# Kernel tuning notes

Measured on AMD Instinct MI355X. Metric: run time of the kernel, lower is better.

## Reference

```python
import jax, jax.numpy as jnp
import numpy as np

K = 512       # knowledge_n = node count AND feature dim
S = 50000     # student_n
E_N = 6       # exer_n (hardcoded as literal 6 in the original forward)
DEG_K = 4     # exercise neighbors per knowledge node
DEG_S = 3     # exercise neighbors per student
NEG_SLOPE = 0.2  # PyG GATConv default


def setup_inputs() -> dict:
    key = jax.random.key(0)
    ks = jax.random.split(key, 10)
    kn_emb = jax.random.normal(ks[0], (K, K), jnp.float32)
    exer_emb = jax.random.normal(ks[1], (E_N, K), jnp.float32)
    all_stu_emb = jax.random.normal(ks[2], (S, K), jnp.float32)
    # k_from_e graph: nodes = [exercises(0..5), knowledge(6..6+K-1)]
    src_ke = jax.random.randint(ks[3], (K * DEG_K,), 0, E_N)
    dst_ke = E_N + jnp.repeat(jnp.arange(K), DEG_K)
    edges_ke = jnp.stack([src_ke, dst_ke]).astype(jnp.int32)   # e -> k
    edges_ek = edges_ke[::-1]                                  # k -> e
    # u_from_e graph: nodes = [exercises(0..5), students(6..6+S-1)]
    src_ue = jax.random.randint(ks[4], (S * DEG_S,), 0, E_N)
    dst_ue = E_N + jnp.repeat(jnp.arange(S), DEG_S)
    edges_ue = jnp.stack([src_ue, dst_ue]).astype(jnp.int32)   # e -> u
    edges_eu = edges_ue[::-1]                                  # u -> e
    sc = 1.0 / np.sqrt(K)
    W_gat = jax.random.normal(ks[5], (4, K, K), jnp.float32) * sc
    a_src = jax.random.normal(ks[6], (4, K), jnp.float32) * sc
    a_dst = jax.random.normal(ks[7], (4, K), jnp.float32) * sc
    b_gat = jnp.zeros((4, K), jnp.float32)
    attn_w = jax.random.normal(ks[8], (3, 2 * K), jnp.float32) / np.sqrt(2 * K)
    attn_b = jnp.zeros((3,), jnp.float32)
    return dict(kn_emb=kn_emb, exer_emb=exer_emb, all_stu_emb=all_stu_emb,
                W_gat=W_gat, a_src=a_src, a_dst=a_dst, b_gat=b_gat,
                attn_w=attn_w, attn_b=attn_b,
                edges_ke=edges_ke, edges_ek=edges_ek,
                edges_ue=edges_ue, edges_eu=edges_eu)


def _gat(x, edges, W, a_s, a_d, b, n):
    """Single-head PyG GATConv with self-loops. edges[0]=src, edges[1]=dst."""
    h = x @ W                                   # [n, K]
    loop = jnp.arange(n, dtype=edges.dtype)
    src = jnp.concatenate([edges[0], loop])
    dst = jnp.concatenate([edges[1], loop])
    alpha_s = h @ a_s                           # [n]
    alpha_d = h @ a_d
    e = jax.nn.leaky_relu(alpha_s[src] + alpha_d[dst], NEG_SLOPE)
    emax = jax.lax.stop_gradient(jax.ops.segment_max(e, dst, num_segments=n))
    ex = jnp.exp(e - emax[dst])
    den = jax.ops.segment_sum(ex, dst, num_segments=n)
    alpha = ex / den[dst]                       # per-dst softmax
    out = jax.ops.segment_sum(alpha[:, None] * h[src], dst, num_segments=n)
    return out + b


def reference(kn_emb, exer_emb, all_stu_emb, W_gat, a_src, a_dst, b_gat,
              attn_w, attn_b, edges_ke, edges_ek, edges_ue, edges_eu):
    e_k = jnp.concatenate([exer_emb, kn_emb], axis=0)        # [6+K, K]
    e_u = jnp.concatenate([exer_emb, all_stu_emb], axis=0)   # [6+S, K]
    n_ek, n_eu = e_k.shape[0], e_u.shape[0]
    k_from_e = _gat(e_k, edges_ke, W_gat[0], a_src[0], a_dst[0], b_gat[0], n_ek)
    e_from_k = _gat(e_k, edges_ek, W_gat[1], a_src[1], a_dst[1], b_gat[1], n_ek)
    u_from_e = _gat(e_u, edges_ue, W_gat[2], a_src[2], a_dst[2], b_gat[2], n_eu)
    e_from_u = _gat(e_u, edges_eu, W_gat[3], a_src[3], a_dst[3], b_gat[3], n_eu)
    # knowledge fusion (softmax over a single column -> all ones, kept faithful)
    D = k_from_e[E_N:]
    s3 = jnp.concatenate([kn_emb, D], axis=1) @ attn_w[0] + attn_b[0]   # [K]
    sc = jax.nn.softmax(s3[:, None], axis=1)
    kn_out = kn_emb + sc[:, 0:1] * D
    # exercise fusion: 2-way attention over knowledge/student messages
    B = e_from_k[:E_N]
    C = e_from_u[:E_N]
    s1 = jnp.concatenate([exer_emb, B], axis=1) @ attn_w[1] + attn_b[1]
    s2 = jnp.concatenate([exer_emb, C], axis=1) @ attn_w[2] + attn_b[2]
    sc2 = jax.nn.softmax(jnp.stack([s1, s2], axis=1), axis=1)           # [6, 2]
    exer_out = exer_emb + sc2[:, 0:1] * B + sc2[:, 1:2] * C
    stu_out = all_stu_emb + u_from_e[E_N:]
    return (kn_out, exer_out, stu_out)
```

## Files before the change

kernel.cpp:

```cpp
#include <hip/hip_runtime.h>

typedef __attribute__((ext_vector_type(4))) float f4;
typedef __attribute__((ext_vector_type(8))) short s8;

__device__ __forceinline__ unsigned short f2bf(float x){
  unsigned u = __float_as_uint(x);
  u += 0x7fffu + ((u >> 16) & 1u);
  return (unsigned short)(u >> 16);
}
__device__ __forceinline__ float lrelu(float v){ return v > 0.f ? v : 0.2f * v; }

__device__ __forceinline__ void gload16(const unsigned short* g, unsigned short* l){
  __builtin_amdgcn_global_load_lds((const __attribute__((address_space(1))) unsigned int*)g,
                                   (__attribute__((address_space(3))) unsigned int*)l, 16, 0, 0);
}

__global__ void prep_pq(const float* __restrict__ Wg, const float* __restrict__ a_src,
                        const float* __restrict__ a_dst, float* __restrict__ pq,
                        float* __restrict__ zbase){
  int tid = blockIdx.x * 256 + threadIdx.x;
  for (int i = tid; i < 6156; i += gridDim.x * 256) zbase[i] = 0.f;
  int wid = tid >> 6, lane = tid & 63;
  for (int task = wid; task < 4096; task += gridDim.x * 4){
    int g = task >> 10, isq = (task >> 9) & 1, r = task & 511;
    const float* w = Wg + ((g * 512 + r) << 9);
    const float* a = (isq ? a_dst : a_src) + g * 512;
    float s = 0.f;
    for (int i = lane; i < 512; i += 64) s += w[i] * a[i];
    for (int off = 32; off; off >>= 1) s += __shfl_down(s, off);
    if (lane == 0) pq[task] = s;
  }
}

__global__ void prep_wt(const float* __restrict__ Wg, unsigned short* __restrict__ W2T,
                        unsigned short* __restrict__ W0T){
  __shared__ float tile[32][33];
  const int b = blockIdx.x;
  const int m = b >> 8;
  const int kb = (b & 15) * 32;
  const int nb = ((b >> 4) & 15) * 32;
  const float* W = Wg + (m == 0 ? 2 * 262144 : 0);
  unsigned short* WT = (m == 0) ? W2T : W0T;
  const int tx = threadIdx.x & 31, ty = threadIdx.x >> 5;
  #pragma unroll
  for (int i = 0; i < 32; i += 8) tile[ty + i][tx] = W[(kb + ty + i) * 512 + nb + tx];
  __syncthreads();
  #pragma unroll
  for (int i = 0; i < 32; i += 8) WT[(nb + ty + i) * 512 + kb + tx] = f2bf(tile[tx][ty + i]);
}

__global__ void prep_he(const float* __restrict__ exer, const float* __restrict__ Wg,
                        const float* __restrict__ pq, float* __restrict__ asE,
                        float* __restrict__ adE, float* __restrict__ HE2,
                        float* __restrict__ HE0){
  const int b = blockIdx.x;
  const int g = (b < 6) ? 0 : 2;
  const int e = b % 6;
  __shared__ float xs[512];
  const int t = threadIdx.x;
  xs[t] = exer[e * 512 + t];
  __syncthreads();
  const int wid = t >> 6, lane = t & 63;
  if (wid < 4){
    int gg = g + (wid >> 1), isq = wid & 1;
    const float* v = pq + gg * 1024 + isq * 512;
    float s = 0.f;
    for (int i = lane; i < 512; i += 64) s += xs[i] * v[i];
    for (int off = 32; off; off >>= 1) s += __shfl_down(s, off);
    if (lane == 0) (isq ? adE : asE)[gg * 6 + e] = s;
  }
  const float* W = Wg + g * 262144;
  float acc = 0.f;
  for (int k = 0; k < 512; k++) acc += xs[k] * W[k * 512 + t];
  ((g == 0) ? HE0 : HE2)[e * 512 + t] = acc;
}

template<int DEG>
__launch_bounds__(256)
__global__ void pass1(const float* __restrict__ x, const float* __restrict__ pq,
                      int gA, int gB,
                      const float* __restrict__ asE, const float* __restrict__ adE,
                      float* __restrict__ alph, const int* __restrict__ idx,
                      float* __restrict__ Craw, float* __restrict__ den, int M)
{
  __shared__ float sC[3072];
  __shared__ float sDen[6];
  const int tid = threadIdx.x, lane = tid & 63, wid = tid >> 6;
  for (int i = tid; i < 3072; i += 256) sC[i] = 0.f;
  if (tid < 6) sDen[tid] = 0.f;

  const int kb = lane * 8;
  const float* pqA = pq + gA * 1024;
  const float* pqB = pq + gB * 1024;
  f4 pA0 = *(const f4*)(pqA + kb),       pA1 = *(const f4*)(pqA + kb + 4);
  f4 qA0 = *(const f4*)(pqA + 512 + kb), qA1 = *(const f4*)(pqA + 512 + kb + 4);
  f4 pB0 = *(const f4*)(pqB + kb),       pB1 = *(const f4*)(pqB + kb + 4);
  float aseR = asE[gA * 6 + (lane % 6)];
  float adeR = adE[gB * 6 + (lane % 6)];

  float cacc[6][8];
  #pragma unroll
  for (int e = 0; e < 6; e++)
    #pragma unroll
    for (int i = 0; i < 8; i++) cacc[e][i] = 0.f;
  float dacc[6] = {0.f,0.f,0.f,0.f,0.f,0.f};
  __syncthreads();

  const int gw = blockIdx.x * 4 + wid, nw = gridDim.x * 4;
  for (int r = gw; r < M; r += nw){
    const float* xr = x + (size_t)r * 512;
    f4 x0 = *(const f4*)(xr + kb), x1 = *(const f4*)(xr + kb + 4);
    float dP = 0.f, dQ = 0.f, dB = 0.f;
    #pragma unroll
    for (int i = 0; i < 4; i++){
      dP += x0[i]*pA0[i] + x1[i]*pA1[i];
      dQ += x0[i]*qA0[i] + x1[i]*qA1[i];
      dB += x0[i]*pB0[i] + x1[i]*pB1[i];
    }
    #pragma unroll
    for (int off = 1; off < 64; off <<= 1){
      dP += __shfl_xor(dP, off); dQ += __shfl_xor(dQ, off); dB += __shfl_xor(dB, off);
    }
    int ei[DEG];
    #pragma unroll
    for (int j = 0; j < DEG; j++) ei[j] = idx[r * DEG + j];
    float scS = lrelu(dP + dQ);
    float sc[DEG], m = scS;
    #pragma unroll
    for (int j = 0; j < DEG; j++){ sc[j] = lrelu(__shfl(aseR, ei[j]) + dQ); m = fmaxf(m, sc[j]); }
    float eS = __expf(scS - m), sum = eS;
    float ev[DEG];
    #pragma unroll
    for (int j = 0; j < DEG; j++){ ev[j] = __expf(sc[j] - m); sum += ev[j]; }
    float inv = 1.f / sum;
    float val = 0.f;
    if (lane == 0) val = eS * inv;
    else if (lane < 7){
      #pragma unroll
      for (int j = 0; j < DEG; j++) val += (ei[j] == lane - 1) ? ev[j] * inv : 0.f;
    }
    if (lane < 8) alph[(size_t)r * 8 + lane] = val;
    float wj[DEG];
    #pragma unroll
    for (int j = 0; j < DEG; j++) wj[j] = __expf(lrelu(dB + __shfl(adeR, ei[j])));
    #pragma unroll
    for (int e = 0; e < 6; e++){
      float we = 0.f;
      #pragma unroll
      for (int j = 0; j < DEG; j++) we += (ei[j] == e) ? wj[j] : 0.f;
      dacc[e] += we;
      #pragma unroll
      for (int i = 0; i < 4; i++){ cacc[e][i] += we * x0[i]; cacc[e][4+i] += we * x1[i]; }
    }
  }
  #pragma unroll
  for (int e = 0; e < 6; e++)
    #pragma unroll
    for (int i = 0; i < 8; i++)
      atomicAdd(&sC[e * 512 + kb + i], cacc[e][i]);
  if (lane == 0){
    #pragma unroll
    for (int e = 0; e < 6; e++) atomicAdd(&sDen[e], dacc[e]);
  }
  __syncthreads();
  for (int i = tid; i < 3072; i += 256){
    float v = sC[i];
    if (v != 0.f) atomicAdd(&Craw[i], v);
  }
  if (tid < 6) atomicAdd(&den[tid], sDen[tid]);
}

__launch_bounds__(256, 2)
__global__ void gemm_ep(const float* __restrict__ x, const unsigned short* __restrict__ WT,
                        const float* __restrict__ alph, const float* __restrict__ HE,
                        const float* __restrict__ bA, float* __restrict__ outp, int M)
{
  __shared__ __align__(16) unsigned short sA[4096];
  __shared__ __align__(16) unsigned short sB[4096];
  __shared__ __align__(16) float sAl[1024];
  __shared__ __align__(16) float sHEb[768];
  __shared__ __align__(16) float sB2[128];

  const int nwg = gridDim.x;
  const int q = nwg >> 3, rr = nwg & 7, xcd = blockIdx.x & 7, pos = blockIdx.x >> 3;
  const int wid = (xcd < rr ? xcd * (q + 1) : rr * (q + 1) + (xcd - rr) * q) + pos;
  const int mb = wid >> 2, nb = wid & 3;
  const int r0 = mb * 128, n0 = nb * 128;
  const int tid = threadIdx.x, lane = tid & 63, w = tid >> 6;
  const int wr = w >> 1, wc = w & 1, l16 = lane & 15, lhi = lane >> 4;

  { int row = min(r0 + (tid >> 1), M - 1);
    *(f4*)(sAl + tid * 4) = *(const f4*)(alph + (size_t)row * 8 + (tid & 1) * 4); }
  if (tid < 192) *(f4*)(sHEb + tid * 4) = *(const f4*)(HE + (tid >> 5) * 512 + n0 + (tid & 31) * 4);
  else if (tid < 224) *(f4*)(sB2 + (tid - 192) * 4) = *(const f4*)(bA + n0 + (tid - 192) * 4);

  const int sRow = tid >> 2, sK = (tid & 3) * 8;
  const float* xA0 = x + (size_t)min(r0 + sRow, M - 1) * 512 + sK;
  const float* xA1 = x + (size_t)min(r0 + 64 + sRow, M - 1) * 512 + sK;
  const unsigned short* gB0 = WT + (size_t)(n0 + sRow) * 512 + sK;
  const unsigned short* gB1 = WT + (size_t)(n0 + 64 + sRow) * 512 + sK;
  unsigned short* lA0 = sA + sRow * 32 + sK;
  unsigned short* lA1 = sA + (64 + sRow) * 32 + sK;
  unsigned short* lB0 = sB + sRow * 32 + sK;
  unsigned short* lB1 = sB + (64 + sRow) * 32 + sK;

  f4 acc[4][4];
  #pragma unroll
  for (int m = 0; m < 4; m++)
    #pragma unroll
    for (int n = 0; n < 4; n++) acc[m][n] = (f4){0.f, 0.f, 0.f, 0.f};

  f4 n00 = *(const f4*)(xA0),     n01 = *(const f4*)(xA0 + 4);
  f4 n10 = *(const f4*)(xA1),     n11 = *(const f4*)(xA1 + 4);

  for (int kt = 0; kt < 16; kt++){
    const int ko = kt * 32;
    gload16(gB0 + ko, lB0);
    gload16(gB1 + ko, lB1);
    s8 p0, p1;
    #pragma unroll
    for (int i = 0; i < 4; i++){
      p0[i]   = (short)f2bf(n00[i]); p0[4+i] = (short)f2bf(n01[i]);
      p1[i]   = (short)f2bf(n10[i]); p1[4+i] = (short)f2bf(n11[i]);
    }
    *(s8*)lA0 = p0; *(s8*)lA1 = p1;
    if (kt < 15){
      n00 = *(const f4*)(xA0 + ko + 32); n01 = *(const f4*)(xA0 + ko + 36);
      n10 = *(const f4*)(xA1 + ko + 32); n11 = *(const f4*)(xA1 + ko + 36);
    }
    __syncthreads();
    s8 af[4], bfr[4];
    #pragma unroll
    for (int m = 0; m < 4; m++) af[m] = *(const s8*)(sA + (wr * 64 + m * 16 + l16) * 32 + lhi * 8);
    #pragma unroll
    for (int n = 0; n < 4; n++) bfr[n] = *(const s8*)(sB + (wc * 64 + n * 16 + l16) * 32 + lhi * 8);
    #pragma unroll
    for (int m = 0; m < 4; m++)
      #pragma unroll
      for (int n = 0; n < 4; n++)
        acc[m][n] = __builtin_amdgcn_mfma_f32_16x16x32_bf16(af[m], bfr[n], acc[m][n], 0, 0, 0);
    __syncthreads();
  }

  #pragma unroll
  for (int m = 0; m < 4; m++){
    const int rl = wr * 64 + m * 16 + lhi * 4;
    #pragma unroll
    for (int n = 0; n < 4; n++){
      const int cl = wc * 64 + n * 16 + l16;
      const int gc = n0 + cl;
      const float hb = sB2[cl];
      #pragma unroll
      for (int j = 0; j < 4; j++){
        const int row = r0 + rl + j;
        if (row < M){
          const float* al = sAl + (rl + j) * 8;
          float v = x[(size_t)row * 512 + gc] + al[0] * acc[m][n][j] + hb;
          #pragma unroll
          for (int e = 0; e < 6; e++) v += al[1 + e] * sHEb[e * 128 + cl];
          outp[(size_t)row * 512 + gc] = v;
        }
      }
    }
  }
}

__global__ void finalize_bc(const float* __restrict__ exer, const float* __restrict__ Wg,
                            const float* __restrict__ asE, const float* __restrict__ adE,
                            const float* __restrict__ Craw3, const float* __restrict__ den3,
                            const float* __restrict__ Craw1, const float* __restrict__ den1,
                            const float* __restrict__ b_gat, float* __restrict__ B,
                            float* __restrict__ C){
  const int b = blockIdx.x;
  const int isC = (b >= 6) ? 1 : 0;
  const int e = b % 6;
  const int g = isC ? 3 : 1;
  const float* Craw = isC ? Craw3 : Craw1;
  const float* den  = isC ? den3  : den1;
  __shared__ float mix[512];
  const int t = threadIdx.x;
  float aS = asE[g*6 + e], aD = adE[g*6 + e];
  float wself = __expf(lrelu(aS + aD));
  float dn = den[e] + wself;
  mix[t] = (Craw[e*512 + t] + wself * exer[e*512 + t]) / dn;
  __syncthreads();
  const float* W = Wg + g * 262144;
  float acc = 0.f;
  for (int k = 0; k < 512; k++) acc += mix[k] * W[k*512 + t];
  acc += b_gat[g*512 + t];
  (isC ? C : B)[e*512 + t] = acc;
}

__global__ void finalize_exer(const float* __restrict__ exer, const float* __restrict__ B,
                              const float* __restrict__ C, const float* __restrict__ attn_w,
                              const float* __restrict__ attn_b, float* __restrict__ outE){
  __shared__ float s1[6], s2[6];
  const int t = threadIdx.x, wid = t >> 6, lane = t & 63;
  for (int task = wid; task < 12; task += 8){
    int e = task >> 1, which = task & 1;
    const float* w = attn_w + (which + 1) * 1024;
    const float* X = exer + e * 512;
    const float* Y = (which ? C : B) + e * 512;
    float s = 0.f;
    for (int i = lane; i < 512; i += 64) s += X[i] * w[i] + Y[i] * w[512 + i];
    for (int off = 32; off; off >>= 1) s += __shfl_down(s, off);
    if (lane == 0) (which ? s2 : s1)[e] = s + attn_b[which + 1];
  }
  __syncthreads();
  for (int i = t; i < 3072; i += 512){
    int e = i >> 9;
    float a = s1[e], b = s2[e];
    float m = fmaxf(a, b);
    float ea = __expf(a - m), eb = __expf(b - m);
    float inv = 1.f / (ea + eb);
    outE[i] = exer[i] + (ea * inv) * B[i] + (eb * inv) * C[i];
  }
}

extern "C" void kernel_launch(void* const* d_in, const int* in_sizes, int n_in,
                              void* d_out, int out_size, void* d_ws, size_t ws_size,
                              hipStream_t stream){
  const float* kn     = (const float*)d_in[0];
  const float* exer   = (const float*)d_in[1];
  const float* stu    = (const float*)d_in[2];
  const float* Wg     = (const float*)d_in[3];
  const float* a_src  = (const float*)d_in[4];
  const float* a_dst  = (const float*)d_in[5];
  const float* b_gat  = (const float*)d_in[6];
  const float* attn_w = (const float*)d_in[7];
  const float* attn_b = (const float*)d_in[8];
  const int*   e_ke   = (const int*)d_in[9];
  const int*   e_ue   = (const int*)d_in[11];
  float* out = (float*)d_out;

  unsigned short* W2T = (unsigned short*)d_ws;
  unsigned short* W0T = W2T + 262144;
  float* pq    = (float*)(W0T + 262144);
  float* asE   = pq + 4096;
  float* adE   = asE + 24;
  float* HE2   = adE + 24;
  float* HE0   = HE2 + 3072;
  float* Craw3 = HE0 + 3072;
  float* Craw1 = Craw3 + 3072;
  float* den3  = Craw1 + 3072;
  float* den1  = den3 + 6;
  float* Bb    = den1 + 6;
  float* Cc    = Bb + 3072;
  float* alphS = Cc + 3072;
  float* alphK = alphS + 400000;

  hipLaunchKernelGGL(prep_pq, dim3(256), dim3(256), 0, stream, Wg, a_src, a_dst, pq, Craw3);
  hipLaunchKernelGGL(prep_wt, dim3(512), dim3(256), 0, stream, Wg, W2T, W0T);
  hipLaunchKernelGGL(prep_he, dim3(12), dim3(512), 0, stream, exer, Wg, pq, asE, adE, HE2, HE0);

  hipLaunchKernelGGL((pass1<3>), dim3(768), dim3(256), 0, stream,
                     stu, pq, 2, 3, asE, adE, alphS, e_ue, Craw3, den3, 50000);
  hipLaunchKernelGGL((pass1<4>), dim3(8), dim3(256), 0, stream,
                     kn, pq, 0, 1, asE, adE, alphK, e_ke, Craw1, den1, 512);

  hipLaunchKernelGGL(gemm_ep, dim3(1564), dim3(256), 0, stream,
                     stu, W2T, alphS, HE2, b_gat + 1024, out + 265216, 50000);
  hipLaunchKernelGGL(gemm_ep, dim3(16), dim3(256), 0, stream,
                     kn, W0T, alphK, HE0, b_gat, out, 512);

  hipLaunchKernelGGL(finalize_bc, dim3(12), dim3(512), 0, stream,
                     exer, Wg, asE, adE, Craw3, den3, Craw1, den1, b_gat, Bb, Cc);
  hipLaunchKernelGGL(finalize_exer, dim3(1), dim3(512), 0, stream,
                     exer, Bb, Cc, attn_w, attn_b, out + 262144);
}
```

Measured before the change: 474.7 us.

## Restructure GEMM to keep full weight tile in LDS and split-K small matvecs

The main GEMM now loads a 64-column slice of the transposed bf16 weight (full K=512) into swizzled LDS once per block. Each of 8 waves streams its own 16 rows of activations straight from global memory, so the per-k-step syncs and the A-tile staging go away. The tile becomes 128x64 with 512 threads. The small exercise matvecs in prep_he and finalize_bc are split across 8 K-chunks with atomic accumulation, and a separate prep_scal kernel computes the attention scalars. The zeroed workspace region is enlarged to cover the new atomic targets. Costs include 64KB of LDS per block limiting occupancy, each activation row being read by 8 column blocks, and atomics that make summation order nondeterministic.

```diff
diff --git a/kernel.cpp b/kernel.cpp
--- a/kernel.cpp
+++ b/kernel.cpp
@@ -19,7 +19,7 @@
                         const float* __restrict__ a_dst, float* __restrict__ pq,
                         float* __restrict__ zbase){
   int tid = blockIdx.x * 256 + threadIdx.x;
-  for (int i = tid; i < 6156; i += gridDim.x * 256) zbase[i] = 0.f;
+  for (int i = tid; i < 18444; i += gridDim.x * 256) zbase[i] = 0.f;
   int wid = tid >> 6, lane = tid & 63;
   for (int task = wid; task < 4096; task += gridDim.x * 4){
     int g = task >> 10, isq = (task >> 9) & 1, r = task & 511;
@@ -49,30 +49,35 @@
   for (int i = 0; i < 32; i += 8) WT[(nb + ty + i) * 512 + kb + tx] = f2bf(tile[tx][ty + i]);
 }
 
+__global__ void prep_scal(const float* __restrict__ exer, const float* __restrict__ pq,
+                          float* __restrict__ asE, float* __restrict__ adE){
+  const int t = threadIdx.x, wid = t >> 6, lane = t & 63;
+  for (int task = wid; task < 48; task += 4){
+    int gg = task / 12, rem = task % 12, isq = rem / 6, e = rem % 6;
+    const float* X = exer + e * 512;
+    const float* V = pq + gg * 1024 + isq * 512;
+    float s = 0.f;
+    for (int i = lane; i < 512; i += 64) s += X[i] * V[i];
+    for (int off = 32; off; off >>= 1) s += __shfl_down(s, off);
+    if (lane == 0) (isq ? adE : asE)[gg * 6 + e] = s;
+  }
+}
+
 __global__ void prep_he(const float* __restrict__ exer, const float* __restrict__ Wg,
-                        const float* __restrict__ pq, float* __restrict__ asE,
-                        float* __restrict__ adE, float* __restrict__ HE2,
-                        float* __restrict__ HE0){
+                        float* __restrict__ HE2, float* __restrict__ HE0){
   const int b = blockIdx.x;
+  const int ks = blockIdx.y;
   const int g = (b < 6) ? 0 : 2;
   const int e = b % 6;
-  __shared__ float xs[512];
+  __shared__ float xs[64];
   const int t = threadIdx.x;
-  xs[t] = exer[e * 512 + t];
-  __syncthreads();
-  const int wid = t >> 6, lane = t & 63;
-  if (wid < 4){
-    int gg = g + (wid >> 1), isq = wid & 1;
-    const float* v = pq + gg * 1024 + isq * 512;
-    float s = 0.f;
-    for (int i = lane; i < 512; i += 64) s += xs[i] * v[i];
-    for (int off = 32; off; off >>= 1) s += __shfl_down(s, off);
-    if (lane == 0) (isq ? adE : asE)[gg * 6 + e] = s;
-  }
-  const float* W = Wg + g * 262144;
+  if (t < 64) xs[t] = exer[e * 512 + ks * 64 + t];
+  __syncthreads();
+  const float* W = Wg + g * 262144 + ks * 64 * 512;
   float acc = 0.f;
-  for (int k = 0; k < 512; k++) acc += xs[k] * W[k * 512 + t];
-  ((g == 0) ? HE0 : HE2)[e * 512 + t] = acc;
+  #pragma unroll 4
+  for (int kk = 0; kk < 64; kk++) acc += xs[kk] * W[kk * 512 + t];
+  atomicAdd(&((g == 0) ? HE0 : HE2)[e * 512 + t], acc);
 }
 
 template<int DEG>
@@ -170,96 +175,91 @@
   if (tid < 6) atomicAdd(&den[tid], sDen[tid]);
 }
 
-__launch_bounds__(256, 2)
+__launch_bounds__(512, 4)
 __global__ void gemm_ep(const float* __restrict__ x, const unsigned short* __restrict__ WT,
                         const float* __restrict__ alph, const float* __restrict__ HE,
                         const float* __restrict__ bA, float* __restrict__ outp, int M)
 {
-  __shared__ __align__(16) unsigned short sA[4096];
-  __shared__ __align__(16) unsigned short sB[4096];
+  __shared__ __align__(16) unsigned short sB[32768];
   __shared__ __align__(16) float sAl[1024];
-  __shared__ __align__(16) float sHEb[768];
-  __shared__ __align__(16) float sB2[128];
+  __shared__ __align__(16) float sHEb[384];
+  __shared__ __align__(16) float sBias[64];
 
   const int nwg = gridDim.x;
-  const int q = nwg >> 3, rr = nwg & 7, xcd = blockIdx.x & 7, pos = blockIdx.x >> 3;
-  const int wid = (xcd < rr ? xcd * (q + 1) : rr * (q + 1) + (xcd - rr) * q) + pos;
-  const int mb = wid >> 2, nb = wid & 3;
-  const int r0 = mb * 128, n0 = nb * 128;
+  const int xcd = blockIdx.x & 7, pos = blockIdx.x >> 3;
+  const int wido = xcd * (nwg >> 3) + pos;
+  const int mb = wido >> 3, nb = wido & 7;
+  const int r0 = mb * 128, n0 = nb * 64;
   const int tid = threadIdx.x, lane = tid & 63, w = tid >> 6;
-  const int wr = w >> 1, wc = w & 1, l16 = lane & 15, lhi = lane >> 4;
-
-  { int row = min(r0 + (tid >> 1), M - 1);
-    *(f4*)(sAl + tid * 4) = *(const f4*)(alph + (size_t)row * 8 + (tid & 1) * 4); }
-  if (tid < 192) *(f4*)(sHEb + tid * 4) = *(const f4*)(HE + (tid >> 5) * 512 + n0 + (tid & 31) * 4);
-  else if (tid < 224) *(f4*)(sB2 + (tid - 192) * 4) = *(const f4*)(bA + n0 + (tid - 192) * 4);
-
-  const int sRow = tid >> 2, sK = (tid & 3) * 8;
-  const float* xA0 = x + (size_t)min(r0 + sRow, M - 1) * 512 + sK;
-  const float* xA1 = x + (size_t)min(r0 + 64 + sRow, M - 1) * 512 + sK;
-  const unsigned short* gB0 = WT + (size_t)(n0 + sRow) * 512 + sK;
-  const unsigned short* gB1 = WT + (size_t)(n0 + 64 + sRow) * 512 + sK;
-  unsigned short* lA0 = sA + sRow * 32 + sK;
-  unsigned short* lA1 = sA + (64 + sRow) * 32 + sK;
-  unsigned short* lB0 = sB + sRow * 32 + sK;
-  unsigned short* lB1 = sB + (64 + sRow) * 32 + sK;
-
-  f4 acc[4][4];
-  #pragma unroll
-  for (int m = 0; m < 4; m++)
-    #pragma unroll
-    for (int n = 0; n < 4; n++) acc[m][n] = (f4){0.f, 0.f, 0.f, 0.f};
-
-  f4 n00 = *(const f4*)(xA0),     n01 = *(const f4*)(xA0 + 4);
-  f4 n10 = *(const f4*)(xA1),     n11 = *(const f4*)(xA1 + 4);
-
+  const int l16 = lane & 15, lhi = lane >> 4;
+
+  {
+    const int row = (tid >> 6), slot = tid & 63;
+    #pragma unroll
+    for (int it = 0; it < 8; it++){
+      const int rr = it * 8 + row;
+      const unsigned short* src = WT + (size_t)(n0 + rr) * 512 + ((slot ^ (rr & 7)) << 3);
+      gload16(src, sB + it * 4096 + tid * 8);
+    }
+  }
+  if (tid < 256){
+    const int row = tid >> 1;
+    *(f4*)(sAl + tid * 4) = *(const f4*)(alph + (size_t)min(r0 + row, M - 1) * 8 + (tid & 1) * 4);
+  } else if (tid < 352){
+    const int idx2 = tid - 256, e = idx2 >> 4, c4 = idx2 & 15;
+    *(f4*)(sHEb + e * 64 + c4 * 4) = *(const f4*)(HE + e * 512 + n0 + c4 * 4);
+  } else if (tid < 368){
+    const int idx2 = tid - 352;
+    *(f4*)(sBias + idx2 * 4) = *(const f4*)(bA + n0 + idx2 * 4);
+  }
+  __syncthreads();
+
+  const int gr0 = r0 + w * 16 + l16;
+  const float* xr = x + (size_t)min(gr0, M - 1) * 512 + lhi * 8;
+
+  f4 acc[4];
+  #pragma unroll
+  for (int n = 0; n < 4; n++) acc[n] = (f4){0.f, 0.f, 0.f, 0.f};
+
+  #pragma unroll 4
   for (int kt = 0; kt < 16; kt++){
-    const int ko = kt * 32;
-    gload16(gB0 + ko, lB0);
-    gload16(gB1 + ko, lB1);
-    s8 p0, p1;
-    #pragma unroll
-    for (int i = 0; i < 4; i++){
-      p0[i]   = (short)f2bf(n00[i]); p0[4+i] = (short)f2bf(n01[i]);
-      p1[i]   = (short)f2bf(n10[i]); p1[4+i] = (short)f2bf(n11[i]);
-    }
-    *(s8*)lA0 = p0; *(s8*)lA1 = p1;
-    if (kt < 15){
-      n00 = *(const f4*)(xA0 + ko + 32); n01 = *(const f4*)(xA0 + ko + 36);
-      n10 = *(const f4*)(xA1 + ko + 32); n11 = *(const f4*)(xA1 + ko + 36);
-    }
-    __syncthreads();
-    s8 af[4], bfr[4];
-    #pragma unroll
-    for (int m = 0; m < 4; m++) af[m] = *(const s8*)(sA + (wr * 64 + m * 16 + l16) * 32 + lhi * 8);
-    #pragma unroll
-    for (int n = 0; n < 4; n++) bfr[n] = *(const s8*)(sB + (wc * 64 + n * 16 + l16) * 32 + lhi * 8);
-    #pragma unroll
-    for (int m = 0; m < 4; m++)
+    f4 a0 = *(const f4*)(xr + kt * 32);
+    f4 a1 = *(const f4*)(xr + kt * 32 + 4);
+    s8 af;
+    #pragma unroll
+    for (int i = 0; i < 4; i++){ af[i] = (short)f2bf(a0[i]); af[4+i] = (short)f2bf(a1[i]); }
+    #pragma unroll
+    for (int n = 0; n < 4; n++){
+      const int row = n * 16 + l16;
+      const int slot = ((kt << 2) + lhi) ^ (row & 7);
+      s8 bf = *(const s8*)(sB + row * 512 + (slot << 3));
+      acc[n] = __builtin_amdgcn_mfma_f32_16x16x32_bf16(af, bf, acc[n], 0, 0, 0);
+    }
+  }
+
+  float hec[4][6], bias[4];
+  #pragma unroll
+  for (int n = 0; n < 4; n++){
+    bias[n] = sBias[n * 16 + l16];
+    #pragma unroll
+    for (int e = 0; e < 6; e++) hec[n][e] = sHEb[e * 64 + n * 16 + l16];
+  }
+
+  #pragma unroll
+  for (int j = 0; j < 4; j++){
+    const int rl = w * 16 + lhi * 4 + j;
+    const int gr = r0 + rl;
+    if (gr < M){
+      f4 alA = *(const f4*)(sAl + rl * 8);
+      f4 alB = *(const f4*)(sAl + rl * 8 + 4);
+      const float aself = alA[0];
       #pragma unroll
-      for (int n = 0; n < 4; n++)
-        acc[m][n] = __builtin_amdgcn_mfma_f32_16x16x32_bf16(af[m], bfr[n], acc[m][n], 0, 0, 0);
-    __syncthreads();
-  }
-
-  #pragma unroll
-  for (int m = 0; m < 4; m++){
-    const int rl = wr * 64 + m * 16 + lhi * 4;
-    #pragma unroll
-    for (int n = 0; n < 4; n++){
-      const int cl = wc * 64 + n * 16 + l16;
-      const int gc = n0 + cl;
-      const float hb = sB2[cl];
-      #pragma unroll
-      for (int j = 0; j < 4; j++){
-        const int row = r0 + rl + j;
-        if (row < M){
-          const float* al = sAl + (rl + j) * 8;
-          float v = x[(size_t)row * 512 + gc] + al[0] * acc[m][n][j] + hb;
-          #pragma unroll
-          for (int e = 0; e < 6; e++) v += al[1 + e] * sHEb[e * 128 + cl];
-          outp[(size_t)row * 512 + gc] = v;
-        }
+      for (int n = 0; n < 4; n++){
+        const int gc = n0 + n * 16 + l16;
+        float v = x[(size_t)gr * 512 + gc] + aself * acc[n][j] + bias[n];
+        v += alA[1] * hec[n][0] + alA[2] * hec[n][1] + alA[3] * hec[n][2];
+        v += alB[0] * hec[n][3] + alB[1] * hec[n][4] + alB[2] * hec[n][5];
+        outp[(size_t)gr * 512 + gc] = v;
       }
     }
   }
@@ -272,23 +272,28 @@
                             const float* __restrict__ b_gat, float* __restrict__ B,
                             float* __restrict__ C){
   const int b = blockIdx.x;
+  const int ks = blockIdx.y;
   const int isC = (b >= 6) ? 1 : 0;
   const int e = b % 6;
   const int g = isC ? 3 : 1;
   const float* Craw = isC ? Craw3 : Craw1;
   const float* den  = isC ? den3  : den1;
-  __shared__ float mix[512];
+  __shared__ float mix[64];
   const int t = threadIdx.x;
   float aS = asE[g*6 + e], aD = adE[g*6 + e];
   float wself = __expf(lrelu(aS + aD));
   float dn = den[e] + wself;
-  mix[t] = (Craw[e*512 + t] + wself * exer[e*512 + t]) / dn;
-  __syncthreads();
-  const float* W = Wg + g * 262144;
+  if (t < 64){
+    int k = ks * 64 + t;
+    mix[t] = (Craw[e*512 + k] + wself * exer[e*512 + k]) / dn;
+  }
+  __syncthreads();
+  const float* W = Wg + g * 262144 + ks * 64 * 512;
   float acc = 0.f;
-  for (int k = 0; k < 512; k++) acc += mix[k] * W[k*512 + t];
-  acc += b_gat[g*512 + t];
-  (isC ? C : B)[e*512 + t] = acc;
+  #pragma unroll 4
+  for (int kk = 0; kk < 64; kk++) acc += mix[kk] * W[kk * 512 + t];
+  if (ks == 0) acc += b_gat[g*512 + t];
+  atomicAdd(&(isC ? C : B)[e*512 + t], acc);
 }
 
 __global__ void finalize_exer(const float* __restrict__ exer, const float* __restrict__ B,
@@ -335,35 +340,37 @@
 
   unsigned short* W2T = (unsigned short*)d_ws;
   unsigned short* W0T = W2T + 262144;
-  float* pq    = (float*)(W0T + 262144);
+  float* fb    = (float*)(W0T + 262144);
+  float* pq    = fb;
   float* asE   = pq + 4096;
   float* adE   = asE + 24;
-  float* HE2   = adE + 24;
-  float* HE0   = HE2 + 3072;
-  float* Craw3 = HE0 + 3072;
+  float* Craw3 = adE + 24;
   float* Craw1 = Craw3 + 3072;
   float* den3  = Craw1 + 3072;
   float* den1  = den3 + 6;
-  float* Bb    = den1 + 6;
+  float* HE2   = den1 + 6;
+  float* HE0   = HE2 + 3072;
+  float* Bb    = HE0 + 3072;
   float* Cc    = Bb + 3072;
   float* alphS = Cc + 3072;
-  float* alphK = alphS + 400000;
+  float* alphK = alphS + 400384;
 
   hipLaunchKernelGGL(prep_pq, dim3(256), dim3(256), 0, stream, Wg, a_src, a_dst, pq, Craw3);
   hipLaunchKernelGGL(prep_wt, dim3(512), dim3(256), 0, stream, Wg, W2T, W0T);
-  hipLaunchKernelGGL(prep_he, dim3(12), dim3(512), 0, stream, exer, Wg, pq, asE, adE, HE2, HE0);
+  hipLaunchKernelGGL(prep_scal, dim3(1), dim3(256), 0, stream, exer, pq, asE, adE);
+  hipLaunchKernelGGL(prep_he, dim3(12, 8), dim3(512), 0, stream, exer, Wg, HE2, HE0);
 
   hipLaunchKernelGGL((pass1<3>), dim3(768), dim3(256), 0, stream,
                      stu, pq, 2, 3, asE, adE, alphS, e_ue, Craw3, den3, 50000);
   hipLaunchKernelGGL((pass1<4>), dim3(8), dim3(256), 0, stream,
                      kn, pq, 0, 1, asE, adE, alphK, e_ke, Craw1, den1, 512);
 
-  hipLaunchKernelGGL(gemm_ep, dim3(1564), dim3(256), 0, stream,
+  hipLaunchKernelGGL(gemm_ep, dim3(391 * 8), dim3(512), 0, stream,
                      stu, W2T, alphS, HE2, b_gat + 1024, out + 265216, 50000);
-  hipLaunchKernelGGL(gemm_ep, dim3(16), dim3(256), 0, stream,
+  hipLaunchKernelGGL(gemm_ep, dim3(4 * 8), dim3(512), 0, stream,
                      kn, W0T, alphK, HE0, b_gat, out, 512);
 
-  hipLaunchKernelGGL(finalize_bc, dim3(12), dim3(512), 0, stream,
+  hipLaunchKernelGGL(finalize_bc, dim3(12, 8), dim3(512), 0, stream,
                      exer, Wg, asE, adE, Craw3, den3, Craw1, den1, b_gat, Bb, Cc);
   hipLaunchKernelGGL(finalize_exer, dim3(1), dim3(512), 0, stream,
                      exer, Bb, Cc, attn_w, attn_b, out + 262144);
```

Result: slower. 485.2 us (+2.2%).

## Merge prep, pass1 and GEMM launches; double-buffer and swizzle GEMM LDS

Applied to the files above, without the earlier changes.

Three prep kernels become one multi-role kernel, the two pass1 launches become one, and the two GEMM launches become one, which cuts launch count from nine to five. The GEMM now double-buffers its A and B tiles with XOR-swizzled LDS offsets, so there is one barrier per k-step and fewer bank conflicts. It also raises occupancy bounds to 3 blocks per CU and hoists the epilogue HE and bias values into registers. Exercise attention scalars are recomputed inside pass1 and fin_bc, and fin_bc is split over K with atomics, which relies on B and C being zeroed by the prep kernel.

```diff
diff --git a/kernel.cpp b/kernel.cpp
--- a/kernel.cpp
+++ b/kernel.cpp
@@ -9,85 +9,77 @@
   return (unsigned short)(u >> 16);
 }
 __device__ __forceinline__ float lrelu(float v){ return v > 0.f ? v : 0.2f * v; }
-
 __device__ __forceinline__ void gload16(const unsigned short* g, unsigned short* l){
   __builtin_amdgcn_global_load_lds((const __attribute__((address_space(1))) unsigned int*)g,
                                    (__attribute__((address_space(3))) unsigned int*)l, 16, 0, 0);
 }
 
-__global__ void prep_pq(const float* __restrict__ Wg, const float* __restrict__ a_src,
-                        const float* __restrict__ a_dst, float* __restrict__ pq,
-                        float* __restrict__ zbase){
-  int tid = blockIdx.x * 256 + threadIdx.x;
-  for (int i = tid; i < 6156; i += gridDim.x * 256) zbase[i] = 0.f;
-  int wid = tid >> 6, lane = tid & 63;
-  for (int task = wid; task < 4096; task += gridDim.x * 4){
-    int g = task >> 10, isq = (task >> 9) & 1, r = task & 511;
-    const float* w = Wg + ((g * 512 + r) << 9);
-    const float* a = (isq ? a_dst : a_src) + g * 512;
+__global__ __launch_bounds__(256) void prep(const float* __restrict__ Wg,
+    const float* __restrict__ a_src, const float* __restrict__ a_dst,
+    const float* __restrict__ exer, float* __restrict__ pq, float* __restrict__ zbase,
+    unsigned short* __restrict__ W2T, unsigned short* __restrict__ W0T,
+    float* __restrict__ HE2, float* __restrict__ HE0)
+{
+  __shared__ float tile[32][33];
+  __shared__ float xs[512];
+  const int b = blockIdx.x, t = threadIdx.x;
+  if (b < 512){
+    const int m = b >> 8, kb = (b & 15) * 32, nb = ((b >> 4) & 15) * 32;
+    const float* W = Wg + (m == 0 ? 2 * 262144 : 0);
+    unsigned short* WT = (m == 0) ? W2T : W0T;
+    const int tx = t & 31, ty = t >> 5;
+    #pragma unroll
+    for (int i = 0; i < 32; i += 8) tile[ty + i][tx] = W[(kb + ty + i) * 512 + nb + tx];
+    __syncthreads();
+    #pragma unroll
+    for (int i = 0; i < 32; i += 8) WT[(nb + ty + i) * 512 + kb + tx] = f2bf(tile[tx][ty + i]);
+  } else if (b < 768){
+    const int tid = (b - 512) * 256 + t;
+    if (tid < 12304) zbase[tid] = 0.f;
+    const int wid = tid >> 6, lane = tid & 63;
+    for (int task = wid; task < 4096; task += 1024){
+      int g = task >> 10, isq = (task >> 9) & 1, r = task & 511;
+      const float* w = Wg + ((g * 512 + r) << 9);
+      const float* a = (isq ? a_dst : a_src) + g * 512;
+      float s = 0.f;
+      for (int i = lane; i < 512; i += 64) s += w[i] * a[i];
+      for (int off = 32; off; off >>= 1) s += __shfl_down(s, off);
+      if (lane == 0) pq[task] = s;
+    }
+  } else {
+    const int b3 = b - 768;
+    const int g = (b3 < 6) ? 0 : 2, e = b3 % 6;
+    xs[t] = exer[e * 512 + t]; xs[t + 256] = exer[e * 512 + 256 + t];
+    __syncthreads();
+    const float* W = Wg + g * 262144;
+    float a0 = 0.f, a1 = 0.f;
+    #pragma unroll 8
+    for (int k = 0; k < 512; k++){ float xv = xs[k]; a0 += xv * W[k * 512 + t]; a1 += xv * W[k * 512 + 256 + t]; }
+    float* HE = (g == 0) ? HE0 : HE2;
+    HE[e * 512 + t] = a0; HE[e * 512 + 256 + t] = a1;
+  }
+}
+
+template<int DEG>
+__device__ void pass1_body(float* sC, float* sDen, float* sASE, float* sADE,
+                           int bid, int nblk, const float* __restrict__ x,
+                           const float* __restrict__ exer, const float* __restrict__ pq,
+                           int gA, int gB, const int* __restrict__ idx,
+                           float* __restrict__ alph, float* __restrict__ Craw,
+                           float* __restrict__ den, int M)
+{
+  const int t = threadIdx.x, lane = t & 63, w = t >> 6;
+  for (int i = t; i < 3072; i += 256) sC[i] = 0.f;
+  if (t < 6) sDen[t] = 0.f;
+  for (int d = w * 3; d < w * 3 + 3; d++){
+    const float* X = exer + (d % 6) * 512;
+    const float* V = (d < 6) ? (pq + gA * 1024) : (pq + gB * 1024 + 512);
     float s = 0.f;
-    for (int i = lane; i < 512; i += 64) s += w[i] * a[i];
+    for (int i = lane; i < 512; i += 64) s += X[i] * V[i];
     for (int off = 32; off; off >>= 1) s += __shfl_down(s, off);
-    if (lane == 0) pq[task] = s;
-  }
-}
-
-__global__ void prep_wt(const float* __restrict__ Wg, unsigned short* __restrict__ W2T,
-                        unsigned short* __restrict__ W0T){
-  __shared__ float tile[32][33];
-  const int b = blockIdx.x;
-  const int m = b >> 8;
-  const int kb = (b & 15) * 32;
-  const int nb = ((b >> 4) & 15) * 32;
-  const float* W = Wg + (m == 0 ? 2 * 262144 : 0);
-  unsigned short* WT = (m == 0) ? W2T : W0T;
-  const int tx = threadIdx.x & 31, ty = threadIdx.x >> 5;
-  #pragma unroll
-  for (int i = 0; i < 32; i += 8) tile[ty + i][tx] = W[(kb + ty + i) * 512 + nb + tx];
-  __syncthreads();
-  #pragma unroll
-  for (int i = 0; i < 32; i += 8) WT[(nb + ty + i) * 512 + kb + tx] = f2bf(tile[tx][ty + i]);
-}
-
-__global__ void prep_he(const float* __restrict__ exer, const float* __restrict__ Wg,
-                        const float* __restrict__ pq, float* __restrict__ asE,
-                        float* __restrict__ adE, float* __restrict__ HE2,
-                        float* __restrict__ HE0){
-  const int b = blockIdx.x;
-  const int g = (b < 6) ? 0 : 2;
-  const int e = b % 6;
-  __shared__ float xs[512];
-  const int t = threadIdx.x;
-  xs[t] = exer[e * 512 + t];
-  __syncthreads();
-  const int wid = t >> 6, lane = t & 63;
-  if (wid < 4){
-    int gg = g + (wid >> 1), isq = wid & 1;
-    const float* v = pq + gg * 1024 + isq * 512;
-    float s = 0.f;
-    for (int i = lane; i < 512; i += 64) s += xs[i] * v[i];
-    for (int off = 32; off; off >>= 1) s += __shfl_down(s, off);
-    if (lane == 0) (isq ? adE : asE)[gg * 6 + e] = s;
-  }
-  const float* W = Wg + g * 262144;
-  float acc = 0.f;
-  for (int k = 0; k < 512; k++) acc += xs[k] * W[k * 512 + t];
-  ((g == 0) ? HE0 : HE2)[e * 512 + t] = acc;
-}
-
-template<int DEG>
-__launch_bounds__(256)
-__global__ void pass1(const float* __restrict__ x, const float* __restrict__ pq,
-                      int gA, int gB,
-                      const float* __restrict__ asE, const float* __restrict__ adE,
-                      float* __restrict__ alph, const int* __restrict__ idx,
-                      float* __restrict__ Craw, float* __restrict__ den, int M)
-{
-  __shared__ float sC[3072];
-  __shared__ float sDen[6];
-  const int tid = threadIdx.x, lane = tid & 63, wid = tid >> 6;
-  for (int i = tid; i < 3072; i += 256) sC[i] = 0.f;
-  if (tid < 6) sDen[tid] = 0.f;
+    if (lane == 0) ((d < 6) ? sASE : sADE)[d % 6] = s;
+  }
+  __syncthreads();
 
   const int kb = lane * 8;
   const float* pqA = pq + gA * 1024;
@@ -95,8 +87,8 @@
   f4 pA0 = *(const f4*)(pqA + kb),       pA1 = *(const f4*)(pqA + kb + 4);
   f4 qA0 = *(const f4*)(pqA + 512 + kb), qA1 = *(const f4*)(pqA + 512 + kb + 4);
   f4 pB0 = *(const f4*)(pqB + kb),       pB1 = *(const f4*)(pqB + kb + 4);
-  float aseR = asE[gA * 6 + (lane % 6)];
-  float adeR = adE[gB * 6 + (lane % 6)];
+  const float aseR = sASE[lane % 6];
+  const float adeR = sADE[lane % 6];
 
   float cacc[6][8];
   #pragma unroll
@@ -104,9 +96,8 @@
     #pragma unroll
     for (int i = 0; i < 8; i++) cacc[e][i] = 0.f;
   float dacc[6] = {0.f,0.f,0.f,0.f,0.f,0.f};
-  __syncthreads();
-
-  const int gw = blockIdx.x * 4 + wid, nw = gridDim.x * 4;
+
+  const int gw = bid * 4 + w, nw = nblk * 4;
   for (int r = gw; r < M; r += nw){
     const float* xr = x + (size_t)r * 512;
     f4 x0 = *(const f4*)(xr + kb), x1 = *(const f4*)(xr + kb + 4);
@@ -163,46 +154,102 @@
     for (int e = 0; e < 6; e++) atomicAdd(&sDen[e], dacc[e]);
   }
   __syncthreads();
-  for (int i = tid; i < 3072; i += 256){
+  for (int i = t; i < 3072; i += 256){
     float v = sC[i];
     if (v != 0.f) atomicAdd(&Craw[i], v);
   }
-  if (tid < 6) atomicAdd(&den[tid], sDen[tid]);
-}
-
-__launch_bounds__(256, 2)
-__global__ void gemm_ep(const float* __restrict__ x, const unsigned short* __restrict__ WT,
-                        const float* __restrict__ alph, const float* __restrict__ HE,
-                        const float* __restrict__ bA, float* __restrict__ outp, int M)
-{
-  __shared__ __align__(16) unsigned short sA[4096];
-  __shared__ __align__(16) unsigned short sB[4096];
+  if (t < 6) atomicAdd(&den[t], sDen[t]);
+}
+
+__global__ __launch_bounds__(256) void pass1_all(const float* __restrict__ stu,
+    const float* __restrict__ kn, const float* __restrict__ exer,
+    const float* __restrict__ pq, const int* __restrict__ e_ue, const int* __restrict__ e_ke,
+    float* __restrict__ alphS, float* __restrict__ alphK,
+    float* __restrict__ Craw3, float* __restrict__ Craw1,
+    float* __restrict__ den3, float* __restrict__ den1)
+{
+  __shared__ float sC[3072];
+  __shared__ float sDen[6], sASE[6], sADE[6];
+  if (blockIdx.x < 768)
+    pass1_body<3>(sC, sDen, sASE, sADE, blockIdx.x, 768, stu, exer, pq, 2, 3,
+                  e_ue, alphS, Craw3, den3, 50000);
+  else
+    pass1_body<4>(sC, sDen, sASE, sADE, blockIdx.x - 768, 8, kn, exer, pq, 0, 1,
+                  e_ke, alphK, Craw1, den1, 512);
+}
+
+__launch_bounds__(256, 3)
+__global__ void gemm_all(const float* __restrict__ stu, const float* __restrict__ kn,
+                         const unsigned short* __restrict__ W2T, const unsigned short* __restrict__ W0T,
+                         const float* __restrict__ alphS, const float* __restrict__ alphK,
+                         const float* __restrict__ HE2, const float* __restrict__ HE0,
+                         const float* __restrict__ b_gat, float* __restrict__ outS,
+                         float* __restrict__ outK)
+{
+  __shared__ __align__(16) unsigned short sA[8192];
+  __shared__ __align__(16) unsigned short sB[8192];
   __shared__ __align__(16) float sAl[1024];
   __shared__ __align__(16) float sHEb[768];
-  __shared__ __align__(16) float sB2[128];
+  __shared__ __align__(16) float sBias[128];
 
   const int nwg = gridDim.x;
-  const int q = nwg >> 3, rr = nwg & 7, xcd = blockIdx.x & 7, pos = blockIdx.x >> 3;
-  const int wid = (xcd < rr ? xcd * (q + 1) : rr * (q + 1) + (xcd - rr) * q) + pos;
-  const int mb = wid >> 2, nb = wid & 3;
+  const int q = nwg >> 3, rr = nwg & 7;
+  const int xcd = blockIdx.x & 7, pos = blockIdx.x >> 3;
+  const int wido = (xcd < rr ? xcd * (q + 1) : rr * (q + 1) + (xcd - rr) * q) + pos;
+
+  const float* x; const unsigned short* WT; const float* alph; const float* HE;
+  const float* bias; float* outp; int M, mb, nb;
+  if (wido < 1564){
+    x = stu; WT = W2T; alph = alphS; HE = HE2; bias = b_gat + 1024; outp = outS; M = 50000;
+    mb = wido >> 2; nb = wido & 3;
+  } else {
+    const int w2 = wido - 1564;
+    x = kn; WT = W0T; alph = alphK; HE = HE0; bias = b_gat; outp = outK; M = 512;
+    mb = w2 >> 2; nb = w2 & 3;
+  }
   const int r0 = mb * 128, n0 = nb * 128;
   const int tid = threadIdx.x, lane = tid & 63, w = tid >> 6;
   const int wr = w >> 1, wc = w & 1, l16 = lane & 15, lhi = lane >> 4;
 
-  { int row = min(r0 + (tid >> 1), M - 1);
-    *(f4*)(sAl + tid * 4) = *(const f4*)(alph + (size_t)row * 8 + (tid & 1) * 4); }
+  const int arow = tid >> 1, akh = (tid & 1) * 16;
+  const float* aptr = x + (size_t)min(r0 + arow, M - 1) * 512 + akh;
+  const int akey = (arow >> 1) & 3, s0 = (tid & 1) * 2;
+  const int dA0 = arow * 32 + ((s0 ^ akey) << 3);
+  const int dA1 = arow * 32 + (((s0 + 1) ^ akey) << 3);
+
+  const int brow = tid >> 2, bslot = tid & 3;
+  const int bkey = (brow >> 1) & 3;
+  const unsigned short* gB0 = WT + (size_t)(n0 + brow) * 512 + ((bslot ^ bkey) << 3);
+  const unsigned short* gB1 = gB0 + (size_t)64 * 512;
+  unsigned short* lB0 = sB + tid * 8;
+  unsigned short* lB1 = sB + 2048 + tid * 8;
+
+  int aoff[4], boff[4];
+  #pragma unroll
+  for (int m = 0; m < 4; m++){
+    const int ra = wr * 64 + m * 16 + l16;
+    aoff[m] = ra * 32 + ((lhi ^ ((ra >> 1) & 3)) << 3);
+    const int rb = wc * 64 + m * 16 + l16;
+    boff[m] = rb * 32 + ((lhi ^ ((rb >> 1) & 3)) << 3);
+  }
+
+  gload16(gB0, lB0); gload16(gB1, lB1);
+  f4 c0 = *(const f4*)(aptr),     c1 = *(const f4*)(aptr + 4);
+  f4 c2 = *(const f4*)(aptr + 8), c3 = *(const f4*)(aptr + 12);
+  {
+    s8 p0, p1;
+    #pragma unroll
+    for (int i = 0; i < 4; i++){
+      p0[i] = (short)f2bf(c0[i]); p0[4+i] = (short)f2bf(c1[i]);
+      p1[i] = (short)f2bf(c2[i]); p1[4+i] = (short)f2bf(c3[i]);
+    }
+    *(s8*)(sA + dA0) = p0; *(s8*)(sA + dA1) = p1;
+  }
+  { const int rw = min(r0 + (tid >> 1), M - 1);
+    *(f4*)(sAl + tid * 4) = *(const f4*)(alph + (size_t)rw * 8 + (tid & 1) * 4); }
   if (tid < 192) *(f4*)(sHEb + tid * 4) = *(const f4*)(HE + (tid >> 5) * 512 + n0 + (tid & 31) * 4);
-  else if (tid < 224) *(f4*)(sB2 + (tid - 192) * 4) = *(const f4*)(bA + n0 + (tid - 192) * 4);
-
-  const int sRow = tid >> 2, sK = (tid & 3) * 8;
-  const float* xA0 = x + (size_t)min(r0 + sRow, M - 1) * 512 + sK;
-  const float* xA1 = x + (size_t)min(r0 + 64 + sRow, M - 1) * 512 + sK;
-  const unsigned short* gB0 = WT + (size_t)(n0 + sRow) * 512 + sK;
-  const unsigned short* gB1 = WT + (size_t)(n0 + 64 + sRow) * 512 + sK;
-  unsigned short* lA0 = sA + sRow * 32 + sK;
-  unsigned short* lA1 = sA + (64 + sRow) * 32 + sK;
-  unsigned short* lB0 = sB + sRow * 32 + sK;
-  unsigned short* lB1 = sB + (64 + sRow) * 32 + sK;
+  else if (tid < 224){ const int i2 = tid - 192; *(f4*)(sBias + i2 * 4) = *(const f4*)(bias + n0 + i2 * 4); }
+  __syncthreads();
 
   f4 acc[4][4];
   #pragma unroll
@@ -210,90 +257,111 @@
     #pragma unroll
     for (int n = 0; n < 4; n++) acc[m][n] = (f4){0.f, 0.f, 0.f, 0.f};
 
-  f4 n00 = *(const f4*)(xA0),     n01 = *(const f4*)(xA0 + 4);
-  f4 n10 = *(const f4*)(xA1),     n11 = *(const f4*)(xA1 + 4);
-
+  int bufo = 0;
+  #pragma unroll 1
   for (int kt = 0; kt < 16; kt++){
-    const int ko = kt * 32;
-    gload16(gB0 + ko, lB0);
-    gload16(gB1 + ko, lB1);
-    s8 p0, p1;
-    #pragma unroll
-    for (int i = 0; i < 4; i++){
-      p0[i]   = (short)f2bf(n00[i]); p0[4+i] = (short)f2bf(n01[i]);
-      p1[i]   = (short)f2bf(n10[i]); p1[4+i] = (short)f2bf(n11[i]);
-    }
-    *(s8*)lA0 = p0; *(s8*)lA1 = p1;
+    const int nxt = bufo ^ 4096;
     if (kt < 15){
-      n00 = *(const f4*)(xA0 + ko + 32); n01 = *(const f4*)(xA0 + ko + 36);
-      n10 = *(const f4*)(xA1 + ko + 32); n11 = *(const f4*)(xA1 + ko + 36);
-    }
-    __syncthreads();
-    s8 af[4], bfr[4];
-    #pragma unroll
-    for (int m = 0; m < 4; m++) af[m] = *(const s8*)(sA + (wr * 64 + m * 16 + l16) * 32 + lhi * 8);
-    #pragma unroll
-    for (int n = 0; n < 4; n++) bfr[n] = *(const s8*)(sB + (wc * 64 + n * 16 + l16) * 32 + lhi * 8);
+      gload16(gB0 + (kt + 1) * 32, lB0 + nxt);
+      gload16(gB1 + (kt + 1) * 32, lB1 + nxt);
+      c0 = *(const f4*)(aptr + (kt + 1) * 32);     c1 = *(const f4*)(aptr + (kt + 1) * 32 + 4);
+      c2 = *(const f4*)(aptr + (kt + 1) * 32 + 8); c3 = *(const f4*)(aptr + (kt + 1) * 32 + 12);
+    }
+    s8 af[4], bf[4];
+    #pragma unroll
+    for (int m = 0; m < 4; m++) af[m] = *(const s8*)(sA + bufo + aoff[m]);
+    #pragma unroll
+    for (int n = 0; n < 4; n++) bf[n] = *(const s8*)(sB + bufo + boff[n]);
     #pragma unroll
     for (int m = 0; m < 4; m++)
       #pragma unroll
       for (int n = 0; n < 4; n++)
-        acc[m][n] = __builtin_amdgcn_mfma_f32_16x16x32_bf16(af[m], bfr[n], acc[m][n], 0, 0, 0);
+        acc[m][n] = __builtin_amdgcn_mfma_f32_16x16x32_bf16(af[m], bf[n], acc[m][n], 0, 0, 0);
+    if (kt < 15){
+      s8 p0, p1;
+      #pragma unroll
+      for (int i = 0; i < 4; i++){
+        p0[i] = (short)f2bf(c0[i]); p0[4+i] = (short)f2bf(c1[i]);
+        p1[i] = (short)f2bf(c2[i]); p1[4+i] = (short)f2bf(c3[i]);
+      }
+      *(s8*)(sA + nxt + dA0) = p0; *(s8*)(sA + nxt + dA1) = p1;
+    }
     __syncthreads();
-  }
-
+    bufo = nxt;
+  }
+
+  float hec[4][6], bi[4];
+  #pragma unroll
+  for (int n = 0; n < 4; n++){
+    const int cl = wc * 64 + n * 16 + l16;
+    bi[n] = sBias[cl];
+    #pragma unroll
+    for (int e = 0; e < 6; e++) hec[n][e] = sHEb[e * 128 + cl];
+  }
   #pragma unroll
   for (int m = 0; m < 4; m++){
-    const int rl = wr * 64 + m * 16 + lhi * 4;
-    #pragma unroll
-    for (int n = 0; n < 4; n++){
-      const int cl = wc * 64 + n * 16 + l16;
-      const int gc = n0 + cl;
-      const float hb = sB2[cl];
-      #pragma unroll
-      for (int j = 0; j < 4; j++){
-        const int row = r0 + rl + j;
-        if (row < M){
-          const float* al = sAl + (rl + j) * 8;
-          float v = x[(size_t)row * 512 + gc] + al[0] * acc[m][n][j] + hb;
-          #pragma unroll
-          for (int e = 0; e < 6; e++) v += al[1 + e] * sHEb[e * 128 + cl];
-          outp[(size_t)row * 512 + gc] = v;
+    #pragma unroll
+    for (int j = 0; j < 4; j++){
+      const int rl = wr * 64 + m * 16 + lhi * 4 + j;
+      const int gr = r0 + rl;
+      if (gr < M){
+        f4 alA = *(const f4*)(sAl + rl * 8);
+        f4 alB = *(const f4*)(sAl + rl * 8 + 4);
+        #pragma unroll
+        for (int n = 0; n < 4; n++){
+          const int gc = n0 + wc * 64 + n * 16 + l16;
+          float v = x[(size_t)gr * 512 + gc] + alA[0] * acc[m][n][j] + bi[n];
+          v += alA[1] * hec[n][0] + alA[2] * hec[n][1] + alA[3] * hec[n][2];
+          v += alB[0] * hec[n][3] + alB[1] * hec[n][4] + alB[2] * hec[n][5];
+          outp[(size_t)gr * 512 + gc] = v;
         }
       }
     }
   }
 }
 
-__global__ void finalize_bc(const float* __restrict__ exer, const float* __restrict__ Wg,
-                            const float* __restrict__ asE, const float* __restrict__ adE,
-                            const float* __restrict__ Craw3, const float* __restrict__ den3,
-                            const float* __restrict__ Craw1, const float* __restrict__ den1,
-                            const float* __restrict__ b_gat, float* __restrict__ B,
-                            float* __restrict__ C){
-  const int b = blockIdx.x;
-  const int isC = (b >= 6) ? 1 : 0;
-  const int e = b % 6;
-  const int g = isC ? 3 : 1;
+__global__ __launch_bounds__(512) void fin_bc(const float* __restrict__ exer,
+    const float* __restrict__ Wg, const float* __restrict__ pq,
+    const float* __restrict__ Craw3, const float* __restrict__ den3,
+    const float* __restrict__ Craw1, const float* __restrict__ den1,
+    const float* __restrict__ b_gat, float* __restrict__ B, float* __restrict__ C)
+{
+  const int b = blockIdx.x, ks = blockIdx.y;
+  const int isC = (b >= 6) ? 1 : 0, e = b % 6, g = isC ? 3 : 1;
   const float* Craw = isC ? Craw3 : Craw1;
   const float* den  = isC ? den3  : den1;
-  __shared__ float mix[512];
-  const int t = threadIdx.x;
-  float aS = asE[g*6 + e], aD = adE[g*6 + e];
-  float wself = __expf(lrelu(aS + aD));
-  float dn = den[e] + wself;
-  mix[t] = (Craw[e*512 + t] + wself * exer[e*512 + t]) / dn;
-  __syncthreads();
-  const float* W = Wg + g * 262144;
+  __shared__ float mix[64];
+  __shared__ float sdots[2];
+  const int t = threadIdx.x, lane = t & 63, w = t >> 6;
+  if (w < 2){
+    const float* V = pq + g * 1024 + w * 512;
+    const float* X = exer + e * 512;
+    float s = 0.f;
+    for (int i = lane; i < 512; i += 64) s += X[i] * V[i];
+    for (int off = 32; off; off >>= 1) s += __shfl_down(s, off);
+    if (lane == 0) sdots[w] = s;
+  }
+  __syncthreads();
+  const float wself = __expf(lrelu(sdots[0] + sdots[1]));
+  const float dn = den[e] + wself;
+  if (t < 64){
+    const int k = ks * 64 + t;
+    mix[t] = (Craw[e * 512 + k] + wself * exer[e * 512 + k]) / dn;
+  }
+  __syncthreads();
+  const float* W = Wg + g * 262144 + ks * 64 * 512;
   float acc = 0.f;
-  for (int k = 0; k < 512; k++) acc += mix[k] * W[k*512 + t];
-  acc += b_gat[g*512 + t];
-  (isC ? C : B)[e*512 + t] = acc;
-}
-
-__global__ void finalize_exer(const float* __restrict__ exer, const float* __restrict__ B,
-                              const float* __restrict__ C, const float* __restrict__ attn_w,
-                              const float* __restrict__ attn_b, float* __restrict__ outE){
+  #pragma unroll 4
+  for (int kk = 0; kk < 64; kk++) acc += mix[kk] * W[kk * 512 + t];
+  if (ks == 0) acc += b_gat[g * 512 + t];
+  atomicAdd(&(isC ? C : B)[e * 512 + t], acc);
+}
+
+__global__ __launch_bounds__(512) void fin_exer(const float* __restrict__ exer,
+    const float* __restrict__ B, const float* __restrict__ C,
+    const float* __restrict__ attn_w, const float* __restrict__ attn_b,
+    float* __restrict__ outE)
+{
   __shared__ float s1[6], s2[6];
   const int t = threadIdx.x, wid = t >> 6, lane = t & 63;
   for (int task = wid; task < 12; task += 8){
@@ -336,35 +404,25 @@
   unsigned short* W2T = (unsigned short*)d_ws;
   unsigned short* W0T = W2T + 262144;
   float* pq    = (float*)(W0T + 262144);
-  float* asE   = pq + 4096;
-  float* adE   = asE + 24;
-  float* HE2   = adE + 24;
-  float* HE0   = HE2 + 3072;
-  float* Craw3 = HE0 + 3072;
+  float* Craw3 = pq + 4096;
   float* Craw1 = Craw3 + 3072;
   float* den3  = Craw1 + 3072;
-  float* den1  = den3 + 6;
-  float* Bb    = den1 + 6;
+  float* den1  = den3 + 8;
+  float* Bb    = den1 + 8;
   float* Cc    = Bb + 3072;
-  float* alphS = Cc + 3072;
-  float* alphK = alphS + 400000;
-
-  hipLaunchKernelGGL(prep_pq, dim3(256), dim3(256), 0, stream, Wg, a_src, a_dst, pq, Craw3);
-  hipLaunchKernelGGL(prep_wt, dim3(512), dim3(256), 0, stream, Wg, W2T, W0T);
-  hipLaunchKernelGGL(prep_he, dim3(12), dim3(512), 0, stream, exer, Wg, pq, asE, adE, HE2, HE0);
-
-  hipLaunchKernelGGL((pass1<3>), dim3(768), dim3(256), 0, stream,
-                     stu, pq, 2, 3, asE, adE, alphS, e_ue, Craw3, den3, 50000);
-  hipLaunchKernelGGL((pass1<4>), dim3(8), dim3(256), 0, stream,
-                     kn, pq, 0, 1, asE, adE, alphK, e_ke, Craw1, den1, 512);
-
-  hipLaunchKernelGGL(gemm_ep, dim3(1564), dim3(256), 0, stream,
-                     stu, W2T, alphS, HE2, b_gat + 1024, out + 265216, 50000);
-  hipLaunchKernelGGL(gemm_ep, dim3(16), dim3(256), 0, stream,
-                     kn, W0T, alphK, HE0, b_gat, out, 512);
-
-  hipLaunchKernelGGL(finalize_bc, dim3(12), dim3(512), 0, stream,
-                     exer, Wg, asE, adE, Craw3, den3, Craw1, den1, b_gat, Bb, Cc);
-  hipLaunchKernelGGL(finalize_exer, dim3(1), dim3(512), 0, stream,
+  float* HE2   = Cc + 3072;
+  float* HE0   = HE2 + 3072;
+  float* alphS = HE0 + 3072;
+  float* alphK = alphS + 400384;
+
+  hipLaunchKernelGGL(prep, dim3(780), dim3(256), 0, stream,
+                     Wg, a_src, a_dst, exer, pq, Craw3, W2T, W0T, HE2, HE0);
+  hipLaunchKernelGGL(pass1_all, dim3(776), dim3(256), 0, stream,
+                     stu, kn, exer, pq, e_ue, e_ke, alphS, alphK, Craw3, Craw1, den3, den1);
+  hipLaunchKernelGGL(gemm_all, dim3(1580), dim3(256), 0, stream,
+                     stu, kn, W2T, W0T, alphS, alphK, HE2, HE0, b_gat, out + 265216, out);
+  hipLaunchKernelGGL(fin_bc, dim3(12, 8), dim3(512), 0, stream,
+                     exer, Wg, pq, Craw3, den3, Craw1, den1, b_gat, Bb, Cc);
+  hipLaunchKernelGGL(fin_exer, dim3(1), dim3(512), 0, stream,
                      exer, Bb, Cc, attn_w, attn_b, out + 262144);
 }
```

Result: faster. 403.2 us (-15.1%).
